# Kernel tuning notes

Hardware: AMD Instinct MI355X
Metric: run time of the kernel (lower is better)

The kernel has to match this reference:

```python
import jax, jax.numpy as jnp
import numpy as np

B, S, D, H, FF = 16, 384, 768, 12, 3072
DH = D // H


def layer_norm(x, g, b, eps=1e-5):
    m = jnp.mean(x, axis=-1, keepdims=True)
    v = jnp.mean((x - m) ** 2, axis=-1, keepdims=True)
    return (x - m) * jax.lax.rsqrt(v + eps) * g + b


def setup_inputs() -> dict:
    key = jax.random.key(0)
    ks = jax.random.split(key, 12)
    s = 0.02
    return {
        "x": jax.random.normal(ks[0], (B, S, D), dtype=jnp.float32),
        "pe": jax.random.normal(ks[1], (2 * S - 1, D), dtype=jnp.float32) * s,  # relative-position table for offsets -(S-1)..(S-1)
        "Wq": jax.random.normal(ks[2], (D, D), dtype=jnp.float32) * s,
        "Wk": jax.random.normal(ks[3], (D, D), dtype=jnp.float32) * s,
        "Wv": jax.random.normal(ks[4], (D, D), dtype=jnp.float32) * s,
        "Wr": jax.random.normal(ks[5], (D, D), dtype=jnp.float32) * s,
        "u": jax.random.normal(ks[6], (H, DH), dtype=jnp.float32) * s,  # content bias (Transformer-XL)
        "v": jax.random.normal(ks[7], (H, DH), dtype=jnp.float32) * s,  # position bias
        "Wo": jax.random.normal(ks[8], (D, D), dtype=jnp.float32) * s,  # attn_ff output projection
        "ln1_g": jnp.ones((D,), dtype=jnp.float32),
        "ln1_b": jnp.zeros((D,), dtype=jnp.float32),
        "ln2_g": jnp.ones((D,), dtype=jnp.float32),
        "ln2_b": jnp.zeros((D,), dtype=jnp.float32),
        "W1": jax.random.normal(ks[9], (D, FF), dtype=jnp.float32) * s,
        "b1": jnp.zeros((FF,), dtype=jnp.float32),
        "W2": jax.random.normal(ks[10], (FF, D), dtype=jnp.float32) * s,
        "b2": jnp.zeros((D,), dtype=jnp.float32),
    }


def reference(x, pe, Wq, Wk, Wv, Wr, u, v, Wo, ln1_g, ln1_b, ln2_g, ln2_b, W1, b1, W2, b2):
    # --- relative-position multi-head self-attention (FLAT / Transformer-XL style) ---
    q = (x @ Wq).reshape(B, S, H, DH)
    k = (x @ Wk).reshape(B, S, H, DH)
    val = (x @ Wv).reshape(B, S, H, DH)
    # project relative table once, then gather per (i, j) offset
    r = (pe @ Wr).reshape(2 * S - 1, H, DH)
    idx = jnp.arange(S)[:, None] - jnp.arange(S)[None, :] + (S - 1)  # [S,S], offset i-j shifted
    rel = r[idx]  # [S,S,H,DH]
    A_C = jnp.einsum("bqhd,bkhd->bhqk", q + u, k)
    B_D = jnp.einsum("bqhd,qkhd->bhqk", q + v, rel)
    scores = (A_C + B_D) * (1.0 / np.sqrt(DH))  # scaled=True
    p = jax.nn.softmax(scores, axis=-1)
    attn = jnp.einsum("bhqk,bkhd->bqhd", p, val).reshape(B, S, D) @ Wo
    # layer_postprocess_sequence = 'an': add residual, then layernorm
    x1 = layer_norm(x + attn, ln1_g, ln1_b)
    # --- FFN (relu) with 'an' postprocess ---
    ff = jax.nn.relu(x1 @ W1 + b1) @ W2 + b2
    return layer_norm(x1 + ff, ln2_g, ln2_b)
```

## Files before the change

### kernel.cpp

```cpp
#include <hip/hip_runtime.h>

typedef unsigned short u16;
typedef __attribute__((ext_vector_type(8))) short short8;
typedef __attribute__((ext_vector_type(4))) float floatx4;

#define B_  16
#define S_  384
#define D_  768
#define H_  12
#define DH_ 64
#define FF_ 3072

__device__ __forceinline__ float b2f(u16 h) { return __uint_as_float(((unsigned)h) << 16); }
__device__ __forceinline__ u16 f2b(float f) {
  unsigned u = __float_as_uint(f);
  u += 0x7fffu + ((u >> 16) & 1u);
  return (u16)(u >> 16);
}

__device__ __forceinline__ void gload16(const u16* g, u16* l) {
  __builtin_amdgcn_global_load_lds(
      (const __attribute__((address_space(1))) unsigned int*)g,
      (__attribute__((address_space(3))) unsigned int*)l, 16, 0, 0);
}

__global__ __launch_bounds__(256) void fill_sentinel(u16* out, int n) {
  int i = blockIdx.x * 256 + threadIdx.x;
  if (i < n) out[i] = 0x42DE;
}

__global__ __launch_bounds__(256) void detect_dtype(const u16* __restrict__ x, int* flag) {
  __shared__ int cnt;
  if (threadIdx.x == 0) cnt = 0;
  __syncthreads();
  int c = 0;
  for (int i = threadIdx.x; i < 8192; i += 256) {
    const unsigned e = (x[i] >> 7) & 0xFFu;
    if (e >= 0xC0u) ++c;
  }
  atomicAdd(&cnt, c);
  __syncthreads();
  if (threadIdx.x == 0) *flag = (cnt > 64) ? 1 : 0;
}

__global__ __launch_bounds__(256) void convert_in4(const void* __restrict__ src,
                                                   u16* __restrict__ dst, int n4,
                                                   const int* __restrict__ flag) {
  const int i = blockIdx.x * 256 + threadIdx.x;
  if (i >= n4) return;
  if (*flag) {
    const float4 f = ((const float4*)src)[i];
    ushort4 o;
    o.x = f2b(f.x); o.y = f2b(f.y); o.z = f2b(f.z); o.w = f2b(f.w);
    ((ushort4*)dst)[i] = o;
  } else {
    ((ushort4*)dst)[i] = ((const ushort4*)src)[i];
  }
}

__global__ __launch_bounds__(256) void convert_small(
    const void* b1, const void* ub, const void* vb, const void* b2,
    const void* g1, const void* be1, const void* g2, const void* be2,
    u16* b1c, u16* ubc, u16* vbc, u16* b2c,
    u16* g1c, u16* be1c, u16* g2c, u16* be2c, const int* __restrict__ flag) {
  const int i = blockIdx.x * 256 + threadIdx.x;
  if (i >= 8448) return;
  const void* s; u16* d; int off;
  if (i < 3072) { s = b1; d = b1c; off = i; }
  else {
    const int r = i - 3072, sg = r / 768; off = r - sg * 768;
    switch (sg) {
      case 0: s = ub;  d = ubc;  break;
      case 1: s = vb;  d = vbc;  break;
      case 2: s = b2;  d = b2c;  break;
      case 3: s = g1;  d = g1c;  break;
      case 4: s = be1; d = be1c; break;
      case 5: s = g2;  d = g2c;  break;
      default: s = be2; d = be2c; break;
    }
  }
  d[off] = (*flag) ? f2b(((const float*)s)[off]) : ((const u16*)s)[off];
}

struct TP { const void* src[7]; u16* dst[7]; };
__global__ __launch_bounds__(256) void transpose_all(TP tp, const int* __restrict__ flag) {
  __shared__ u16 t[32][33];
  const int f32 = *flag;
  const int id = blockIdx.x;
  int w, tt, R, C, bc, br;
  if (id < 2880)      { w = id / 576; tt = id % 576;  R = 768;  C = 768;  bc = (tt % 24) * 32; br = (tt / 24) * 32; }
  else if (id < 5184) { w = 5;        tt = id - 2880; R = 768;  C = 3072; bc = (tt % 96) * 32; br = (tt / 96) * 32; }
  else                { w = 6;        tt = id - 5184; R = 3072; C = 768;  bc = (tt % 24) * 32; br = (tt / 24) * 32; }
  const void* in = tp.src[w];
  u16* out = tp.dst[w];
  const int tx = threadIdx.x & 31, ty = threadIdx.x >> 5;
  for (int i = ty; i < 32; i += 8) {
    const size_t idx = (size_t)(br + i) * C + bc + tx;
    t[i][tx] = f32 ? f2b(((const float*)in)[idx]) : ((const u16*)in)[idx];
  }
  __syncthreads();
  for (int i = ty; i < 32; i += 8) out[(size_t)(bc + i) * R + br + tx] = t[tx][i];
}

enum { F_BIAS = 1, F_RELU = 2, F_RES = 4, F_QKV = 8 };

template <int TM, int TN, int WM, int WN, int FLAGS>
__global__ __launch_bounds__(256) void gemm3(
    const u16* __restrict__ A, const u16* __restrict__ Bt,
    u16* __restrict__ out0, u16* __restrict__ out1,
    u16* __restrict__ out2, u16* __restrict__ out3,
    const u16* __restrict__ bias0, const u16* __restrict__ bias1,
    const u16* __restrict__ res, int M, int N, int K) {
  constexpr int WAVES_M = TM / WM;
  constexpr int MT = WM / 16, NT = WN / 16;
  constexpr int NI = (TM + TN) / 64;
  static_assert((TM / WM) * (TN / WN) == 4, "4 waves");
  __shared__ u16 SM[2][(TM + TN) * 32];

  const int m0 = blockIdx.y * TM;
  const int n0 = blockIdx.x * TN;
  const int tid = threadIdx.x;
  const int wid = tid >> 6, lane = tid & 63;
  const int wm = (wid % WAVES_M) * WM, wn = (wid / WAVES_M) * WN;
  const int lm = lane & 15, quad = lane >> 4;

  floatx4 acc[MT][NT];
#pragma unroll
  for (int i = 0; i < MT; ++i)
#pragma unroll
    for (int j = 0; j < NT; ++j) acc[i][j] = (floatx4){0.f, 0.f, 0.f, 0.f};

  const u16* srcs[NI];
  int ldso[NI];
#pragma unroll
  for (int i = 0; i < NI; ++i) {
    const int j = wid + 4 * i;
    const int r = j * 16 + (lane >> 2);
    const int q = (lane & 3) ^ ((r >> 1) & 3);
    const u16* p;
    if (r < TM) {
      int ga = m0 + r;
      if (ga > M - 1) ga = M - 1;
      p = A + (size_t)ga * K + q * 8;
    } else {
      p = Bt + (size_t)(n0 + r - TM) * K + q * 8;
    }
    srcs[i] = p;
    ldso[i] = j * 512;
  }
  const int slot = (quad ^ ((lm >> 1) & 3)) * 8;
  int aoff[MT], boff[NT];
#pragma unroll
  for (int t = 0; t < MT; ++t) aoff[t] = (wm + t * 16 + lm) * 32 + slot;
#pragma unroll
  for (int t = 0; t < NT; ++t) boff[t] = (TM + wn + t * 16 + lm) * 32 + slot;

#pragma unroll
  for (int i = 0; i < NI; ++i) gload16(srcs[i], &SM[0][ldso[i]]);
  __syncthreads();

  int buf = 0;
  for (int k0 = 0; k0 < K; k0 += 32, buf ^= 1) {
    if (k0 + 32 < K) {
      const int koff = (k0 + 32);
#pragma unroll
      for (int i = 0; i < NI; ++i) gload16(srcs[i] + koff, &SM[buf ^ 1][ldso[i]]);
    }
    short8 af[MT], bf[NT];
#pragma unroll
    for (int t = 0; t < MT; ++t) af[t] = *(const short8*)(&SM[buf][aoff[t]]);
#pragma unroll
    for (int t = 0; t < NT; ++t) bf[t] = *(const short8*)(&SM[buf][boff[t]]);
#pragma unroll
    for (int tm = 0; tm < MT; ++tm)
#pragma unroll
      for (int tn = 0; tn < NT; ++tn)
        acc[tm][tn] = __builtin_amdgcn_mfma_f32_16x16x32_bf16(af[tm], bf[tn], acc[tm][tn], 0, 0, 0);
    __syncthreads();
  }

#pragma unroll
  for (int tm = 0; tm < MT; ++tm) {
#pragma unroll
    for (int tn = 0; tn < NT; ++tn) {
      const int gcol = n0 + wn + tn * 16 + lm;
#pragma unroll
      for (int r = 0; r < 4; ++r) {
        const int grow = m0 + wm + tm * 16 + quad * 4 + r;
        if (grow >= M) continue;
        float val = acc[tm][tn][r];
        if (FLAGS & F_QKV) {
          const int region = gcol / 768;
          const int c = gcol - region * 768;
          if (region == 0) {
            out0[(size_t)grow * 768 + c] = f2b(val + b2f(bias0[c]));
            out1[(size_t)grow * 768 + c] = f2b(val + b2f(bias1[c]));
          } else if (region == 1) {
            out2[(size_t)grow * 768 + c] = f2b(val);
          } else {
            const int bb = grow / S_, s = grow - bb * S_;
            out3[((size_t)bb * D_ + c) * S_ + s] = f2b(val);
          }
        } else {
          if (FLAGS & F_BIAS) val += b2f(bias0[gcol]);
          if (FLAGS & F_RES) val += b2f(res[(size_t)grow * N + gcol]);
          if (FLAGS & F_RELU) val = fmaxf(val, 0.f);
          out0[(size_t)grow * N + gcol] = f2b(val);
        }
      }
    }
  }
}

__global__ __launch_bounds__(512, 4) void attn_kernel(
    const u16* __restrict__ qu, const u16* __restrict__ qv,
    const u16* __restrict__ kb, const u16* __restrict__ vt,
    const u16* __restrict__ rb, u16* __restrict__ attn) {
  __shared__ float scA[32 * 396];
  __shared__ u16 Eb[32 * 424];
  __shared__ float rsum[32];

  const int id = blockIdx.x;
  const int g = id >> 3;
  const int qt = g % 12;
  const int bh = (id & 7) + 8 * (g / 12);
  const int b = bh / H_, h = bh % H_;
  const int i0 = qt * 32;
  const int tid = threadIdx.x, wid = tid >> 6, lane = tid & 63;
  const int lm = lane & 15, quad = lane >> 4;

  const size_t qr0 = ((size_t)(b * S_ + i0 + lm)) * D_ + h * DH_;
  const size_t qr1 = qr0 + (size_t)16 * D_;
  const short8 qv0a = *(const short8*)(qv + qr0 + quad * 8);
  const short8 qv0b = *(const short8*)(qv + qr0 + 32 + quad * 8);
  const short8 qv1a = *(const short8*)(qv + qr1 + quad * 8);
  const short8 qv1b = *(const short8*)(qv + qr1 + 32 + quad * 8);
  const short8 qu0a = *(const short8*)(qu + qr0 + quad * 8);
  const short8 qu0b = *(const short8*)(qu + qr0 + 32 + quad * 8);
  const short8 qu1a = *(const short8*)(qu + qr1 + quad * 8);
  const short8 qu1b = *(const short8*)(qu + qr1 + 32 + quad * 8);

#pragma unroll
  for (int i = 0; i < 7; ++i) {
    const int u = wid + 8 * i;
    if (u >= 50) break;
    if (u < 26) {
      const int m = u;
      int t = i0 + 16 * m + lm;
      if (t > 766) t = 766;
      const u16* p = rb + (size_t)t * D_ + h * DH_;
      const short8 b0 = *(const short8*)(p + quad * 8);
      const short8 b1 = *(const short8*)(p + 32 + quad * 8);
      if (m <= 24) {
        floatx4 e = (floatx4){0.f, 0.f, 0.f, 0.f};
        e = __builtin_amdgcn_mfma_f32_16x16x32_bf16(qv0a, b0, e, 0, 0, 0);
        e = __builtin_amdgcn_mfma_f32_16x16x32_bf16(qv0b, b1, e, 0, 0, 0);
#pragma unroll
        for (int r = 0; r < 4; ++r) Eb[(quad * 4 + r) * 424 + 16 * m + lm] = f2b(e[r]);
      }
      if (m >= 1) {
        floatx4 e = (floatx4){0.f, 0.f, 0.f, 0.f};
        e = __builtin_amdgcn_mfma_f32_16x16x32_bf16(qv1a, b0, e, 0, 0, 0);
        e = __builtin_amdgcn_mfma_f32_16x16x32_bf16(qv1b, b1, e, 0, 0, 0);
#pragma unroll
        for (int r = 0; r < 4; ++r) Eb[(16 + quad * 4 + r) * 424 + 16 * (m - 1) + lm] = f2b(e[r]);
      }
    } else {
      const int j = u - 26;
      const u16* p = kb + ((size_t)(b * S_ + j * 16 + lm)) * D_ + h * DH_;
      const short8 b0 = *(const short8*)(p + quad * 8);
      const short8 b1 = *(const short8*)(p + 32 + quad * 8);
      floatx4 e0 = (floatx4){0.f, 0.f, 0.f, 0.f};
      e0 = __builtin_amdgcn_mfma_f32_16x16x32_bf16(qu0a, b0, e0, 0, 0, 0);
      e0 = __builtin_amdgcn_mfma_f32_16x16x32_bf16(qu0b, b1, e0, 0, 0, 0);
      floatx4 e1 = (floatx4){0.f, 0.f, 0.f, 0.f};
      e1 = __builtin_amdgcn_mfma_f32_16x16x32_bf16(qu1a, b0, e1, 0, 0, 0);
      e1 = __builtin_amdgcn_mfma_f32_16x16x32_bf16(qu1b, b1, e1, 0, 0, 0);
#pragma unroll
      for (int r = 0; r < 4; ++r) {
        scA[(quad * 4 + r) * 396 + j * 16 + lm] = e0[r];
        scA[(16 + quad * 4 + r) * 396 + j * 16 + lm] = e1[r];
      }
    }
  }
  __syncthreads();

  u16* p16 = (u16*)scA;
  {
    const int row = wid * 4 + quad;
    const int rbase = row * 424 + (row & 15) + 383;
    float v[24];
    float lmax = -1e30f;
#pragma unroll
    for (int cc = 0; cc < 24; ++cc) {
      const int c = lm + cc * 16;
      const float s = (scA[row * 396 + c] + b2f(Eb[rbase - c])) * 0.125f;
      v[cc] = s;
      lmax = fmaxf(lmax, s);
    }
#pragma unroll
    for (int m = 1; m < 16; m <<= 1) lmax = fmaxf(lmax, __shfl_xor(lmax, m));
    float lsum = 0.f;
#pragma unroll
    for (int cc = 0; cc < 24; ++cc) {
      const float e = __expf(v[cc] - lmax);
      p16[row * 792 + lm + cc * 16] = f2b(e);
      lsum += e;
    }
#pragma unroll
    for (int m = 1; m < 16; m <<= 1) lsum += __shfl_xor(lsum, m);
    if (lm == 0) rsum[row] = lsum;
  }
  __syncthreads();

  {
    const int rg = wid & 1, nt = wid >> 1;
    floatx4 o = (floatx4){0.f, 0.f, 0.f, 0.f};
    const size_t vbase = ((size_t)(b * D_ + h * DH_ + nt * 16 + lm)) * S_;
    const int pbase = (rg * 16 + lm) * 792;
#pragma unroll
    for (int kk = 0; kk < 12; ++kk) {
      const short8 af = *(const short8*)(&p16[pbase + kk * 32 + quad * 8]);
      const short8 bv = *(const short8*)(vt + vbase + kk * 32 + quad * 8);
      o = __builtin_amdgcn_mfma_f32_16x16x32_bf16(af, bv, o, 0, 0, 0);
    }
#pragma unroll
    for (int r = 0; r < 4; ++r) {
      const int row = rg * 16 + quad * 4 + r;
      attn[((size_t)(b * S_ + i0 + row)) * D_ + h * DH_ + nt * 16 + lm] =
          f2b(o[r] / rsum[row]);
    }
  }
}

__global__ __launch_bounds__(256) void ln_kernel(const u16* __restrict__ y,
                                                 const u16* __restrict__ g,
                                                 const u16* __restrict__ bb,
                                                 void* __restrict__ outv,
                                                 const int* __restrict__ flag, int dual) {
  const int row = blockIdx.x * 4 + (threadIdx.x >> 6);
  const int lane = threadIdx.x & 63;
  const u16* yr = y + (size_t)row * D_;
  float vbuf[12], s = 0.f, s2 = 0.f;
#pragma unroll
  for (int i = 0; i < 12; ++i) {
    const float x = b2f(yr[lane + i * 64]);
    vbuf[i] = x;
    s += x;
    s2 += x * x;
  }
#pragma unroll
  for (int off = 32; off; off >>= 1) {
    s += __shfl_down(s, off);
    s2 += __shfl_down(s2, off);
  }
  s = __shfl(s, 0);
  s2 = __shfl(s2, 0);
  const float mean = s * (1.f / 768.f);
  const float var = s2 * (1.f / 768.f) - mean * mean;
  const float inv = rsqrtf(var + 1e-5f);
  const int f32out = dual && *flag;
#pragma unroll
  for (int i = 0; i < 12; ++i) {
    const int c = lane + i * 64;
    const float val = (vbuf[i] - mean) * inv * b2f(g[c]) + b2f(bb[c]);
    if (f32out) ((float*)outv)[(size_t)row * D_ + c] = val;
    else ((u16*)outv)[(size_t)row * D_ + c] = f2b(val);
  }
}

extern "C" void kernel_launch(void* const* d_in, const int* in_sizes, int n_in,
                              void* d_out, int out_size, void* d_ws, size_t ws_size,
                              hipStream_t stream) {
  const void* x    = d_in[0];
  const void* pe   = d_in[1];
  const void* Wq   = d_in[2];
  const void* Wk   = d_in[3];
  const void* Wv   = d_in[4];
  const void* Wr   = d_in[5];
  const void* ub   = d_in[6];
  const void* vb   = d_in[7];
  const void* Wo   = d_in[8];
  const void* ln1g = d_in[9];
  const void* ln1b = d_in[10];
  const void* ln2g = d_in[11];
  const void* ln2b = d_in[12];
  const void* W1   = d_in[13];
  const void* b1   = d_in[14];
  const void* W2   = d_in[15];
  const void* b2   = d_in[16];
  char* ws = (char*)d_ws;

  constexpr int N_X  = B_ * S_ * D_;
  constexpr int N_PE = (2 * S_ - 1) * D_;

  constexpr size_t O_W   = 0;
  constexpr size_t O_SM  = 15335424;
  constexpr size_t O_XB  = 15368192;
  constexpr size_t O_QU  = 24805376;
  constexpr size_t O_QV  = 34242560;
  constexpr size_t O_KB  = 43679744;
  constexpr size_t O_VT  = 53116928;
  constexpr size_t O_RB  = 62554112;
  constexpr size_t NEEDED = 63733760;

  if (ws_size < NEEDED) {
    fill_sentinel<<<(out_size + 255) / 256, 256, 0, stream>>>((u16*)d_out, out_size);
    return;
  }

  int* flag = (int*)(ws + O_SM);
  u16* ubc  = (u16*)(ws + O_SM + 128);
  u16* vbc  = (u16*)(ws + O_SM + 1664);
  u16* b1c  = (u16*)(ws + O_SM + 3200);
  u16* b2c  = (u16*)(ws + O_SM + 9344);
  u16* g1c  = (u16*)(ws + O_SM + 10880);
  u16* be1c = (u16*)(ws + O_SM + 12416);
  u16* g2c  = (u16*)(ws + O_SM + 13952);
  u16* be2c = (u16*)(ws + O_SM + 15488);

  u16* wtq = (u16*)(ws + O_W);
  u16* wtk = wtq + (size_t)D_ * D_;
  u16* wtv = wtk + (size_t)D_ * D_;
  u16* wtr = wtv + (size_t)D_ * D_;
  u16* wto = wtr + (size_t)D_ * D_;
  u16* wt1 = wto + (size_t)D_ * D_;
  u16* wt2 = wt1 + (size_t)D_ * FF_;

  u16* xb  = (u16*)(ws + O_XB);
  u16* quB = (u16*)(ws + O_QU);
  u16* peb = (u16*)(ws + O_QV);
  u16* qvB = (u16*)(ws + O_QV);
  u16* kbB = (u16*)(ws + O_KB);
  u16* vtB = (u16*)(ws + O_VT);
  u16* rbB = (u16*)(ws + O_RB);
  u16* atB = (u16*)d_out;
  u16* y1B = xb;
  u16* x1B = (u16*)(ws + O_VT);
  u16* ffB = xb;
  u16* y2B = x1B;

  detect_dtype<<<1, 256, 0, stream>>>((const u16*)x, flag);
  convert_in4<<<(N_X / 4 + 255) / 256, 256, 0, stream>>>(x, xb, N_X / 4, flag);
  convert_in4<<<(N_PE / 4 + 255) / 256, 256, 0, stream>>>(pe, peb, N_PE / 4, flag);
  convert_small<<<33, 256, 0, stream>>>(b1, ub, vb, b2, ln1g, ln1b, ln2g, ln2b,
                                        b1c, ubc, vbc, b2c, g1c, be1c, g2c, be2c, flag);
  TP tp;
  tp.src[0] = Wq; tp.src[1] = Wk; tp.src[2] = Wv; tp.src[3] = Wr; tp.src[4] = Wo;
  tp.src[5] = W1; tp.src[6] = W2;
  tp.dst[0] = wtq; tp.dst[1] = wtk; tp.dst[2] = wtv; tp.dst[3] = wtr; tp.dst[4] = wto;
  tp.dst[5] = wt1; tp.dst[6] = wt2;
  transpose_all<<<7488, 256, 0, stream>>>(tp, flag);

  gemm3<64, 64, 32, 32, 0><<<dim3(12, 12), 256, 0, stream>>>(
      peb, wtr, rbB, nullptr, nullptr, nullptr, nullptr, nullptr, nullptr,
      2 * S_ - 1, D_, D_);
  gemm3<128, 128, 64, 64, F_QKV><<<dim3(18, 48), 256, 0, stream>>>(
      xb, wtq, quB, qvB, kbB, vtB, ubc, vbc, nullptr, B_ * S_, 2304, D_);
  attn_kernel<<<2304, 512, 0, stream>>>(quB, qvB, kbB, vtB, rbB, atB);
  gemm3<64, 128, 32, 64, F_RES><<<dim3(6, 96), 256, 0, stream>>>(
      atB, wto, y1B, nullptr, nullptr, nullptr, nullptr, nullptr, xb, B_ * S_, D_, D_);
  ln_kernel<<<B_ * S_ / 4, 256, 0, stream>>>(y1B, g1c, be1c, x1B, flag, 0);
  gemm3<128, 128, 64, 64, F_BIAS | F_RELU><<<dim3(24, 48), 256, 0, stream>>>(
      x1B, wt1, ffB, nullptr, nullptr, nullptr, b1c, nullptr, nullptr, B_ * S_, FF_, D_);
  gemm3<64, 128, 32, 64, F_BIAS | F_RES><<<dim3(6, 96), 256, 0, stream>>>(
      ffB, wt2, y2B, nullptr, nullptr, nullptr, b2c, nullptr, x1B, B_ * S_, D_, FF_);
  ln_kernel<<<B_ * S_ / 4, 256, 0, stream>>>(y2B, g2c, be2c, d_out, flag, 1);
}
```

Baseline: 459.5 us.

## Merge preamble kernels and fuse rel-pos GEMM into QKV launch with transposed V store

Folds dtype detection, input conversions, small-parameter conversion and weight transposes into a single preamble launch, with each block detecting the dtype itself via a ballot. The relative-position projection GEMM is merged into the QKV GEMM launch as extra tiles, and the V-transpose epilogue now stages through shared memory so it can write 16-byte vectors instead of scattered 2-byte stores. The intent is fewer kernel launches, better GPU fill, and coalesced V^T writes. It also changes dtype detection to an any-lane threshold and places the pe buffer in the output region.

```diff
diff --git a/kernel.cpp b/kernel.cpp
--- a/kernel.cpp
+++ b/kernel.cpp
@@ -29,87 +29,95 @@
   if (i < n) out[i] = 0x42DE;
 }
 
-__global__ __launch_bounds__(256) void detect_dtype(const u16* __restrict__ x, int* flag) {
-  __shared__ int cnt;
-  if (threadIdx.x == 0) cnt = 0;
+__device__ __forceinline__ int detect_flag(const u16* x, int tid, int* sh) {
+  const unsigned e = (x[tid] >> 7) & 0xFFu;
+  const unsigned long long m = __ballot(e >= 0xC0u);
+  if ((tid & 63) == 0) sh[tid >> 6] = (m != 0ull) ? 1 : 0;
   __syncthreads();
-  int c = 0;
-  for (int i = threadIdx.x; i < 8192; i += 256) {
-    const unsigned e = (x[i] >> 7) & 0xFFu;
-    if (e >= 0xC0u) ++c;
-  }
-  atomicAdd(&cnt, c);
-  __syncthreads();
-  if (threadIdx.x == 0) *flag = (cnt > 64) ? 1 : 0;
-}
-
-__global__ __launch_bounds__(256) void convert_in4(const void* __restrict__ src,
-                                                   u16* __restrict__ dst, int n4,
-                                                   const int* __restrict__ flag) {
-  const int i = blockIdx.x * 256 + threadIdx.x;
-  if (i >= n4) return;
-  if (*flag) {
-    const float4 f = ((const float4*)src)[i];
-    ushort4 o;
-    o.x = f2b(f.x); o.y = f2b(f.y); o.z = f2b(f.z); o.w = f2b(f.w);
-    ((ushort4*)dst)[i] = o;
-  } else {
-    ((ushort4*)dst)[i] = ((const ushort4*)src)[i];
-  }
-}
-
-__global__ __launch_bounds__(256) void convert_small(
+  return sh[0] | sh[1] | sh[2] | sh[3];
+}
+
+struct TP { const void* src[7]; u16* dst[7]; };
+__global__ __launch_bounds__(256) void preamble_all(
+    TP tp, const void* x, const void* pe,
     const void* b1, const void* ub, const void* vb, const void* b2,
     const void* g1, const void* be1, const void* g2, const void* be2,
+    u16* xb, u16* peb,
     u16* b1c, u16* ubc, u16* vbc, u16* b2c,
-    u16* g1c, u16* be1c, u16* g2c, u16* be2c, const int* __restrict__ flag) {
-  const int i = blockIdx.x * 256 + threadIdx.x;
-  if (i >= 8448) return;
-  const void* s; u16* d; int off;
-  if (i < 3072) { s = b1; d = b1c; off = i; }
-  else {
-    const int r = i - 3072, sg = r / 768; off = r - sg * 768;
-    switch (sg) {
-      case 0: s = ub;  d = ubc;  break;
-      case 1: s = vb;  d = vbc;  break;
-      case 2: s = b2;  d = b2c;  break;
-      case 3: s = g1;  d = g1c;  break;
-      case 4: s = be1; d = be1c; break;
-      case 5: s = g2;  d = g2c;  break;
-      default: s = be2; d = be2c; break;
-    }
-  }
-  d[off] = (*flag) ? f2b(((const float*)s)[off]) : ((const u16*)s)[off];
-}
-
-struct TP { const void* src[7]; u16* dst[7]; };
-__global__ __launch_bounds__(256) void transpose_all(TP tp, const int* __restrict__ flag) {
+    u16* g1c, u16* be1c, u16* g2c, u16* be2c, int* flag_ws) {
   __shared__ u16 t[32][33];
-  const int f32 = *flag;
+  __shared__ int fl[4];
+  const int tid = threadIdx.x;
+  const int f32 = detect_flag((const u16*)x, tid, fl);
   const int id = blockIdx.x;
-  int w, tt, R, C, bc, br;
-  if (id < 2880)      { w = id / 576; tt = id % 576;  R = 768;  C = 768;  bc = (tt % 24) * 32; br = (tt / 24) * 32; }
-  else if (id < 5184) { w = 5;        tt = id - 2880; R = 768;  C = 3072; bc = (tt % 96) * 32; br = (tt / 96) * 32; }
-  else                { w = 6;        tt = id - 5184; R = 3072; C = 768;  bc = (tt % 24) * 32; br = (tt / 24) * 32; }
-  const void* in = tp.src[w];
-  u16* out = tp.dst[w];
-  const int tx = threadIdx.x & 31, ty = threadIdx.x >> 5;
-  for (int i = ty; i < 32; i += 8) {
-    const size_t idx = (size_t)(br + i) * C + bc + tx;
-    t[i][tx] = f32 ? f2b(((const float*)in)[idx]) : ((const u16*)in)[idx];
-  }
-  __syncthreads();
-  for (int i = ty; i < 32; i += 8) out[(size_t)(bc + i) * R + br + tx] = t[tx][i];
-}
-
-enum { F_BIAS = 1, F_RELU = 2, F_RES = 4, F_QKV = 8 };
+  if (id == 0 && tid == 0) *flag_ws = f32;
+
+  if (id < 7488) {
+    int w, tt, R, C, bc, br;
+    if (id < 2880)      { w = id / 576; tt = id % 576;  R = 768;  C = 768;  bc = (tt % 24) * 32; br = (tt / 24) * 32; }
+    else if (id < 5184) { w = 5;        tt = id - 2880; R = 768;  C = 3072; bc = (tt % 96) * 32; br = (tt / 96) * 32; }
+    else                { w = 6;        tt = id - 5184; R = 3072; C = 768;  bc = (tt % 24) * 32; br = (tt / 24) * 32; }
+    const void* in = tp.src[w];
+    u16* out = tp.dst[w];
+    const int tx = tid & 31, ty = tid >> 5;
+    for (int i = ty; i < 32; i += 8) {
+      const size_t idx = (size_t)(br + i) * C + bc + tx;
+      t[i][tx] = f32 ? f2b(((const float*)in)[idx]) : ((const u16*)in)[idx];
+    }
+    __syncthreads();
+    for (int i = ty; i < 32; i += 8) out[(size_t)(bc + i) * R + br + tx] = t[tx][i];
+  } else if (id < 12096) {
+    const int i = (id - 7488) * 256 + tid;
+    if (i < B_ * S_ * D_ / 4) {
+      if (f32) {
+        const float4 f = ((const float4*)x)[i];
+        ushort4 o;
+        o.x = f2b(f.x); o.y = f2b(f.y); o.z = f2b(f.z); o.w = f2b(f.w);
+        ((ushort4*)xb)[i] = o;
+      } else {
+        ((ushort4*)xb)[i] = ((const ushort4*)x)[i];
+      }
+    }
+  } else if (id < 12672) {
+    const int i = (id - 12096) * 256 + tid;
+    if (i < (2 * S_ - 1) * D_ / 4) {
+      if (f32) {
+        const float4 f = ((const float4*)pe)[i];
+        ushort4 o;
+        o.x = f2b(f.x); o.y = f2b(f.y); o.z = f2b(f.z); o.w = f2b(f.w);
+        ((ushort4*)peb)[i] = o;
+      } else {
+        ((ushort4*)peb)[i] = ((const ushort4*)pe)[i];
+      }
+    }
+  } else {
+    const int i = (id - 12672) * 256 + tid;
+    if (i < 8448) {
+      const void* s; u16* d; int off;
+      if (i < 3072) { s = b1; d = b1c; off = i; }
+      else {
+        const int r = i - 3072, sg = r / 768; off = r - sg * 768;
+        switch (sg) {
+          case 0: s = ub;  d = ubc;  break;
+          case 1: s = vb;  d = vbc;  break;
+          case 2: s = b2;  d = b2c;  break;
+          case 3: s = g1;  d = g1c;  break;
+          case 4: s = be1; d = be1c; break;
+          case 5: s = g2;  d = g2c;  break;
+          default: s = be2; d = be2c; break;
+        }
+      }
+      d[off] = f32 ? f2b(((const float*)s)[off]) : ((const u16*)s)[off];
+    }
+  }
+}
+
+enum { F_BIAS = 1, F_RELU = 2, F_RES = 4 };
 
 template <int TM, int TN, int WM, int WN, int FLAGS>
 __global__ __launch_bounds__(256) void gemm3(
     const u16* __restrict__ A, const u16* __restrict__ Bt,
-    u16* __restrict__ out0, u16* __restrict__ out1,
-    u16* __restrict__ out2, u16* __restrict__ out3,
-    const u16* __restrict__ bias0, const u16* __restrict__ bias1,
+    u16* __restrict__ out0, const u16* __restrict__ bias0,
     const u16* __restrict__ res, int M, int N, int K) {
   constexpr int WAVES_M = TM / WM;
   constexpr int MT = WM / 16, NT = WN / 16;
@@ -189,23 +197,147 @@
         const int grow = m0 + wm + tm * 16 + quad * 4 + r;
         if (grow >= M) continue;
         float val = acc[tm][tn][r];
-        if (FLAGS & F_QKV) {
-          const int region = gcol / 768;
-          const int c = gcol - region * 768;
-          if (region == 0) {
-            out0[(size_t)grow * 768 + c] = f2b(val + b2f(bias0[c]));
-            out1[(size_t)grow * 768 + c] = f2b(val + b2f(bias1[c]));
-          } else if (region == 1) {
-            out2[(size_t)grow * 768 + c] = f2b(val);
-          } else {
-            const int bb = grow / S_, s = grow - bb * S_;
-            out3[((size_t)bb * D_ + c) * S_ + s] = f2b(val);
-          }
+        if (FLAGS & F_BIAS) val += b2f(bias0[gcol]);
+        if (FLAGS & F_RES) val += b2f(res[(size_t)grow * N + gcol]);
+        if (FLAGS & F_RELU) val = fmaxf(val, 0.f);
+        out0[(size_t)grow * N + gcol] = f2b(val);
+      }
+    }
+  }
+}
+
+__global__ __launch_bounds__(256) void gemm_qkv_rp(
+    const u16* __restrict__ xb, const u16* __restrict__ wqkv,
+    const u16* __restrict__ peb, const u16* __restrict__ wtr,
+    u16* __restrict__ qu, u16* __restrict__ qv,
+    u16* __restrict__ kbo, u16* __restrict__ vto, u16* __restrict__ rbo,
+    const u16* __restrict__ ubias, const u16* __restrict__ vbias) {
+  constexpr int TM = 128, TN = 128, WM = 64, WN = 64;
+  constexpr int MT = 4, NT = 4, NI = 4;
+  __shared__ u16 SM[2][(TM + TN) * 32];
+
+  const int id = blockIdx.x;
+  const int qkv = (id < 864) ? 1 : 0;
+  int bx, by, M, N;
+  const u16 *A, *Bt;
+  if (qkv) { bx = id % 18; by = id / 18; M = B_ * S_; N = 2304; A = xb; Bt = wqkv; }
+  else     { const int t2 = id - 864; bx = t2 % 6; by = t2 / 6; M = 767; N = 768; A = peb; Bt = wtr; }
+  const int K = 768;
+  const int m0 = by * TM, n0 = bx * TN;
+  const int tid = threadIdx.x;
+  const int wid = tid >> 6, lane = tid & 63;
+  const int wm = (wid & 1) * WM, wn = (wid >> 1) * WN;
+  const int lm = lane & 15, quad = lane >> 4;
+
+  floatx4 acc[MT][NT];
+#pragma unroll
+  for (int i = 0; i < MT; ++i)
+#pragma unroll
+    for (int j = 0; j < NT; ++j) acc[i][j] = (floatx4){0.f, 0.f, 0.f, 0.f};
+
+  const u16* srcs[NI];
+  int ldso[NI];
+#pragma unroll
+  for (int i = 0; i < NI; ++i) {
+    const int j = wid + 4 * i;
+    const int r = j * 16 + (lane >> 2);
+    const int q = (lane & 3) ^ ((r >> 1) & 3);
+    const u16* p;
+    if (r < TM) {
+      int ga = m0 + r;
+      if (ga > M - 1) ga = M - 1;
+      p = A + (size_t)ga * K + q * 8;
+    } else {
+      p = Bt + (size_t)(n0 + r - TM) * K + q * 8;
+    }
+    srcs[i] = p;
+    ldso[i] = j * 512;
+  }
+  const int slot = (quad ^ ((lm >> 1) & 3)) * 8;
+  int aoff[MT], boff[NT];
+#pragma unroll
+  for (int t = 0; t < MT; ++t) aoff[t] = (wm + t * 16 + lm) * 32 + slot;
+#pragma unroll
+  for (int t = 0; t < NT; ++t) boff[t] = (TM + wn + t * 16 + lm) * 32 + slot;
+
+#pragma unroll
+  for (int i = 0; i < NI; ++i) gload16(srcs[i], &SM[0][ldso[i]]);
+  __syncthreads();
+
+  int buf = 0;
+  for (int k0 = 0; k0 < K; k0 += 32, buf ^= 1) {
+    if (k0 + 32 < K) {
+      const int koff = (k0 + 32);
+#pragma unroll
+      for (int i = 0; i < NI; ++i) gload16(srcs[i] + koff, &SM[buf ^ 1][ldso[i]]);
+    }
+    short8 af[MT], bf[NT];
+#pragma unroll
+    for (int t = 0; t < MT; ++t) af[t] = *(const short8*)(&SM[buf][aoff[t]]);
+#pragma unroll
+    for (int t = 0; t < NT; ++t) bf[t] = *(const short8*)(&SM[buf][boff[t]]);
+#pragma unroll
+    for (int tm = 0; tm < MT; ++tm)
+#pragma unroll
+      for (int tn = 0; tn < NT; ++tn)
+        acc[tm][tn] = __builtin_amdgcn_mfma_f32_16x16x32_bf16(af[tm], bf[tn], acc[tm][tn], 0, 0, 0);
+    __syncthreads();
+  }
+
+  if (!qkv) {
+#pragma unroll
+    for (int tm = 0; tm < MT; ++tm)
+#pragma unroll
+      for (int tn = 0; tn < NT; ++tn) {
+        const int gcol = n0 + wn + tn * 16 + lm;
+#pragma unroll
+        for (int r = 0; r < 4; ++r) {
+          const int grow = m0 + wm + tm * 16 + quad * 4 + r;
+          if (grow < M) rbo[(size_t)grow * 768 + gcol] = f2b(acc[tm][tn][r]);
+        }
+      }
+    return;
+  }
+  const int region = n0 / 768;
+  if (region == 2) {
+    u16* wbuf = &SM[0][0] + wid * 1088;
+    const int bb = (m0 + wm) / S_;
+    const int sbase = (m0 + wm) % S_;
+    const int cl = lane >> 2, sc = (lane & 3) * 16;
+#pragma unroll
+    for (int tn = 0; tn < NT; ++tn) {
+#pragma unroll
+      for (int tm = 0; tm < MT; ++tm)
+#pragma unroll
+        for (int r = 0; r < 4; ++r)
+          wbuf[(tm * 16 + quad * 4 + r) * 17 + lm] = f2b(acc[tm][tn][r]);
+      short8 s0, s1;
+#pragma unroll
+      for (int j = 0; j < 8; ++j) s0[j] = (short)wbuf[(sc + j) * 17 + cl];
+#pragma unroll
+      for (int j = 0; j < 8; ++j) s1[j] = (short)wbuf[(sc + 8 + j) * 17 + cl];
+      const int cglob = n0 - 1536 + wn + tn * 16 + cl;
+      u16* dst = vto + ((size_t)(bb * D_ + cglob)) * S_ + sbase + sc;
+      *(short8*)dst = s0;
+      *(short8*)(dst + 8) = s1;
+    }
+    return;
+  }
+#pragma unroll
+  for (int tm = 0; tm < MT; ++tm) {
+#pragma unroll
+    for (int tn = 0; tn < NT; ++tn) {
+      const int gcol = n0 + wn + tn * 16 + lm;
+      const int c = gcol - region * 768;
+#pragma unroll
+      for (int r = 0; r < 4; ++r) {
+        const int grow = m0 + wm + tm * 16 + quad * 4 + r;
+        const float val = acc[tm][tn][r];
+        if (region == 0) {
+          qu[(size_t)grow * 768 + c] = f2b(val + b2f(ubias[c]));
+          qv[(size_t)grow * 768 + c] = f2b(val + b2f(vbias[c]));
         } else {
-          if (FLAGS & F_BIAS) val += b2f(bias0[gcol]);
-          if (FLAGS & F_RES) val += b2f(res[(size_t)grow * N + gcol]);
-          if (FLAGS & F_RELU) val = fmaxf(val, 0.f);
-          out0[(size_t)grow * N + gcol] = f2b(val);
+          kbo[(size_t)grow * 768 + c] = f2b(val);
         }
       }
     }
@@ -240,10 +372,7 @@
   const short8 qu1a = *(const short8*)(qu + qr1 + quad * 8);
   const short8 qu1b = *(const short8*)(qu + qr1 + 32 + quad * 8);
 
-#pragma unroll
-  for (int i = 0; i < 7; ++i) {
-    const int u = wid + 8 * i;
-    if (u >= 50) break;
+  for (int u = wid; u < 50; u += 8) {
     if (u < 26) {
       const int m = u;
       int t = i0 + 16 * m + lm;
@@ -391,9 +520,6 @@
   const void* b2   = d_in[16];
   char* ws = (char*)d_ws;
 
-  constexpr int N_X  = B_ * S_ * D_;
-  constexpr int N_PE = (2 * S_ - 1) * D_;
-
   constexpr size_t O_W   = 0;
   constexpr size_t O_SM  = 15335424;
   constexpr size_t O_XB  = 15368192;
@@ -429,41 +555,35 @@
 
   u16* xb  = (u16*)(ws + O_XB);
   u16* quB = (u16*)(ws + O_QU);
-  u16* peb = (u16*)(ws + O_QV);
   u16* qvB = (u16*)(ws + O_QV);
   u16* kbB = (u16*)(ws + O_KB);
   u16* vtB = (u16*)(ws + O_VT);
   u16* rbB = (u16*)(ws + O_RB);
+  u16* peb = (u16*)d_out;
   u16* atB = (u16*)d_out;
   u16* y1B = xb;
   u16* x1B = (u16*)(ws + O_VT);
   u16* ffB = xb;
   u16* y2B = x1B;
 
-  detect_dtype<<<1, 256, 0, stream>>>((const u16*)x, flag);
-  convert_in4<<<(N_X / 4 + 255) / 256, 256, 0, stream>>>(x, xb, N_X / 4, flag);
-  convert_in4<<<(N_PE / 4 + 255) / 256, 256, 0, stream>>>(pe, peb, N_PE / 4, flag);
-  convert_small<<<33, 256, 0, stream>>>(b1, ub, vb, b2, ln1g, ln1b, ln2g, ln2b,
-                                        b1c, ubc, vbc, b2c, g1c, be1c, g2c, be2c, flag);
   TP tp;
   tp.src[0] = Wq; tp.src[1] = Wk; tp.src[2] = Wv; tp.src[3] = Wr; tp.src[4] = Wo;
   tp.src[5] = W1; tp.src[6] = W2;
   tp.dst[0] = wtq; tp.dst[1] = wtk; tp.dst[2] = wtv; tp.dst[3] = wtr; tp.dst[4] = wto;
   tp.dst[5] = wt1; tp.dst[6] = wt2;
-  transpose_all<<<7488, 256, 0, stream>>>(tp, flag);
-
-  gemm3<64, 64, 32, 32, 0><<<dim3(12, 12), 256, 0, stream>>>(
-      peb, wtr, rbB, nullptr, nullptr, nullptr, nullptr, nullptr, nullptr,
-      2 * S_ - 1, D_, D_);
-  gemm3<128, 128, 64, 64, F_QKV><<<dim3(18, 48), 256, 0, stream>>>(
-      xb, wtq, quB, qvB, kbB, vtB, ubc, vbc, nullptr, B_ * S_, 2304, D_);
+
+  preamble_all<<<12705, 256, 0, stream>>>(tp, x, pe, b1, ub, vb, b2, ln1g, ln1b,
+                                          ln2g, ln2b, xb, peb, b1c, ubc, vbc, b2c,
+                                          g1c, be1c, g2c, be2c, flag);
+  gemm_qkv_rp<<<900, 256, 0, stream>>>(xb, wtq, peb, wtr, quB, qvB, kbB, vtB, rbB,
+                                       ubc, vbc);
   attn_kernel<<<2304, 512, 0, stream>>>(quB, qvB, kbB, vtB, rbB, atB);
   gemm3<64, 128, 32, 64, F_RES><<<dim3(6, 96), 256, 0, stream>>>(
-      atB, wto, y1B, nullptr, nullptr, nullptr, nullptr, nullptr, xb, B_ * S_, D_, D_);
+      atB, wto, y1B, nullptr, xb, B_ * S_, D_, D_);
   ln_kernel<<<B_ * S_ / 4, 256, 0, stream>>>(y1B, g1c, be1c, x1B, flag, 0);
   gemm3<128, 128, 64, 64, F_BIAS | F_RELU><<<dim3(24, 48), 256, 0, stream>>>(
-      x1B, wt1, ffB, nullptr, nullptr, nullptr, b1c, nullptr, nullptr, B_ * S_, FF_, D_);
+      x1B, wt1, ffB, b1c, nullptr, B_ * S_, FF_, D_);
   gemm3<64, 128, 32, 64, F_BIAS | F_RES><<<dim3(6, 96), 256, 0, stream>>>(
-      ffB, wt2, y2B, nullptr, nullptr, nullptr, b2c, nullptr, x1B, B_ * S_, D_, FF_);
+      ffB, wt2, y2B, b2c, x1B, B_ * S_, D_, FF_);
   ln_kernel<<<B_ * S_ / 4, 256, 0, stream>>>(y2B, g2c, be2c, d_out, flag, 1);
 }
```

Result: faster. 426.9 us (-7.1%).
